# Kernel tuning notes

Hardware: AMD Instinct MI355X
Metric: run time of the kernel (lower is better)

## Reference

```python
import jax, jax.numpy as jnp
import numpy as np
import math

B, NQ, NK = 32, 1024, 1024
DQ = DK = DV = 512
H = 8
EPS = 1e-5


def _layernorm(x, g, b):
    mu = jnp.mean(x, axis=-1, keepdims=True)
    var = jnp.mean(jnp.square(x - mu), axis=-1, keepdims=True)
    return (x - mu) * jax.lax.rsqrt(var + EPS) * g + b


def setup_inputs() -> dict:
    key = jax.random.key(0)
    ks = jax.random.split(key, 8)
    s = 0.03  # small init scale for linear weights
    return {
        "Q": jax.random.normal(ks[0], (B, NQ, DQ), jnp.float32),
        "K": jax.random.normal(ks[1], (B, NK, DK), jnp.float32),
        "Wq": jax.random.normal(ks[2], (DQ, DV), jnp.float32) * s,
        "bq": jnp.zeros((DV,), jnp.float32),
        "Wk": jax.random.normal(ks[3], (DK, DV), jnp.float32) * s,
        "bk": jnp.zeros((DV,), jnp.float32),
        "Wv": jax.random.normal(ks[4], (DK, DV), jnp.float32) * s,
        "bv": jnp.zeros((DV,), jnp.float32),
        "Wo": jax.random.normal(ks[5], (DV, DV), jnp.float32) * s,
        "bo": jnp.zeros((DV,), jnp.float32),
        "g0": jnp.ones((DV,), jnp.float32),
        "beta0": jnp.zeros((DV,), jnp.float32),
        "g1": jnp.ones((DV,), jnp.float32),
        "beta1": jnp.zeros((DV,), jnp.float32),
    }


def reference(Q, K, Wq, bq, Wk, bk, Wv, bv, Wo, bo, g0, beta0, g1, beta1):
    b, nq, _ = Q.shape
    nk = K.shape[1]
    d = DV // H  # head dim (dim_split)

    q = Q @ Wq + bq            # [B, Nq, DV]
    k = K @ Wk + bk            # [B, Nk, DV]
    v = K @ Wv + bv            # [B, Nk, DV]

    # torch.cat(x.split(d, 2), 0) == reshape to [B,N,H,d] then stack heads on batch dim
    qh = q.reshape(b, nq, H, d).transpose(2, 0, 1, 3)  # [H, B, Nq, d]
    kh = k.reshape(b, nk, H, d).transpose(2, 0, 1, 3)  # [H, B, Nk, d]
    vh = v.reshape(b, nk, H, d).transpose(2, 0, 1, 3)  # [H, B, Nk, d]

    # NOTE: scaled by sqrt(dim_V), and softmax over the QUERY axis (torch dim=1)
    scores = jnp.einsum('hbqd,hbkd->hbqk', qh, kh) / math.sqrt(DV)
    A = jax.nn.softmax(scores, axis=2)                 # over Nq (faithful to source)
    oh = qh + jnp.einsum('hbqk,hbkd->hbqd', A, vh)     # residual on Q_

    out = oh.transpose(1, 2, 0, 3).reshape(b, nq, DV)  # merge heads back
    out = _layernorm(out, g0, beta0)
    out = out + jax.nn.relu(out @ Wo + bo)
    out = _layernorm(out, g1, beta1)
    return out
```

## Files before the change

kernel.cpp:

```cpp
#include <hip/hip_runtime.h>

#define Bz  32
#define NQz 1024
#define NKz 1024
#define SCALE 0.04419417382415922f

typedef __bf16 bf16_t;
typedef bf16_t bf16x8 __attribute__((ext_vector_type(8)));
typedef bf16_t bf16x4 __attribute__((ext_vector_type(4)));
typedef float  f32x4  __attribute__((ext_vector_type(4)));

#define MFMA16(a, b, c) __builtin_amdgcn_mfma_f32_16x16x32_bf16(a, b, c, 0, 0, 0)

__global__ __launch_bounds__(256) void cvt_bf16(const float* __restrict__ Q,
                                                const float* __restrict__ K,
                                                bf16_t* __restrict__ Qb,
                                                bf16_t* __restrict__ Kb) {
  const size_t i = ((size_t)blockIdx.x * 256 + threadIdx.x) * 8;
  const float* src = blockIdx.y ? K : Q;
  bf16_t* dst = blockIdx.y ? Kb : Qb;
  float4 a = *(const float4*)(src + i);
  float4 b = *(const float4*)(src + i + 4);
  bf16x8 r;
  r[0] = (bf16_t)a.x; r[1] = (bf16_t)a.y; r[2] = (bf16_t)a.z; r[3] = (bf16_t)a.w;
  r[4] = (bf16_t)b.x; r[5] = (bf16_t)b.y; r[6] = (bf16_t)b.z; r[7] = (bf16_t)b.w;
  *(bf16x8*)(dst + i) = r;
}

__global__ void transpose_w(const float* __restrict__ W0, const float* __restrict__ W1,
                            const float* __restrict__ W2, const float* __restrict__ W3,
                            bf16_t* __restrict__ out) {
  __shared__ float tile[32][33];
  const float* W = blockIdx.z == 0 ? W0 : blockIdx.z == 1 ? W1 : blockIdx.z == 2 ? W2 : W3;
  bf16_t* o = out + (size_t)blockIdx.z * 512 * 512;
  const int n0 = blockIdx.x * 32, k0 = blockIdx.y * 32;
  const int tx = threadIdx.x, ty = threadIdx.y;
  for (int i = 0; i < 4; i++)
    tile[ty + i * 8][tx] = W[(size_t)(k0 + ty + i * 8) * 512 + n0 + tx];
  __syncthreads();
  for (int i = 0; i < 4; i++)
    o[(size_t)(n0 + ty + i * 8) * 512 + k0 + tx] = (bf16_t)tile[tx][ty + i * 8];
}

template <int MODE>
__global__ __launch_bounds__(256) void gemm_k(const bf16_t* __restrict__ A,
                                              const bf16_t* __restrict__ Wt,
                                              const float* __restrict__ bias, float mult,
                                              bf16_t* __restrict__ C) {
  __shared__ __align__(16) bf16_t As[128][40];
  __shared__ __align__(16) bf16_t Bs[128][40];
  const int t = threadIdx.x;
  const int wave = t >> 6, lane = t & 63;
  const int quad = lane >> 4, l16 = lane & 15;
  const int wm = wave & 1, wn = wave >> 1;
  const int m0 = blockIdx.x * 128, n0 = blockIdx.y * 128;
  const int r = t >> 1, half = t & 1;

  f32x4 acc[4][4] = {};

  for (int k0 = 0; k0 < 512; k0 += 32) {
    __syncthreads();
    {
      const bf16_t* ap = A + (size_t)(m0 + r) * 512 + k0 + half * 16;
      *(bf16x8*)&As[r][half * 16 + 0] = *(const bf16x8*)(ap + 0);
      *(bf16x8*)&As[r][half * 16 + 8] = *(const bf16x8*)(ap + 8);
      const bf16_t* bp = Wt + (size_t)(n0 + r) * 512 + k0 + half * 16;
      *(bf16x8*)&Bs[r][half * 16 + 0] = *(const bf16x8*)(bp + 0);
      *(bf16x8*)&Bs[r][half * 16 + 8] = *(const bf16x8*)(bp + 8);
    }
    __syncthreads();
    bf16x8 af[4], bfv[4];
    for (int mt = 0; mt < 4; mt++)
      af[mt] = *(const bf16x8*)&As[wm * 64 + mt * 16 + l16][quad * 8];
    for (int nt = 0; nt < 4; nt++)
      bfv[nt] = *(const bf16x8*)&Bs[wn * 64 + nt * 16 + l16][quad * 8];
    for (int mt = 0; mt < 4; mt++)
      for (int nt = 0; nt < 4; nt++)
        acc[mt][nt] = MFMA16(af[mt], bfv[nt], acc[mt][nt]);
  }

  for (int mt = 0; mt < 4; mt++) {
    for (int nt = 0; nt < 4; nt++) {
      const int row = m0 + wm * 64 + mt * 16 + quad * 4;
      const int col = n0 + wn * 64 + nt * 16 + l16;
      const float bv = bias[col];
      for (int rg = 0; rg < 4; rg++) {
        float v = acc[mt][nt][rg] + bv;
        if (MODE == 0) {
          C[(size_t)(row + rg) * 512 + col] = (bf16_t)(v * mult);
        } else {
          float x = (float)A[(size_t)(row + rg) * 512 + col];
          C[(size_t)(row + rg) * 512 + col] = (bf16_t)(x + fmaxf(v, 0.f));
        }
      }
    }
  }
}

__global__ __launch_bounds__(256) void attn_stats(const bf16_t* __restrict__ qp,
                                                  const bf16_t* __restrict__ kp,
                                                  const bf16_t* __restrict__ vp,
                                                  bf16_t* __restrict__ Vt) {
  __shared__ __align__(16) bf16_t Vs[128][72];
  __shared__ __align__(16) bf16_t Qs[64][72];
  __shared__ float ls[128];
  const int t = threadIdx.x;
  const int wave = t >> 6, lane = t & 63;
  const int quad = lane >> 4, l16 = lane & 15;
  const int id = blockIdx.x;
  const int kb = ((id >> 3) & 7) * 128;
  const int hb = (id & 7) * 32 + (id >> 6);
  const int h = hb >> 5, b = hb & 31;
  const bf16_t* qbase = qp + (size_t)b * NQz * 512 + h * 64;
  const bf16_t* kbase = kp + (size_t)b * NKz * 512 + h * 64;

  {
    const int r = t >> 1, half = t & 1;
    const bf16_t* vr = vp + (size_t)b * NKz * 512 + (size_t)(kb + r) * 512 + h * 64 + half * 32;
    *(bf16x8*)&Vs[r][half * 32 + 0]  = *(const bf16x8*)(vr + 0);
    *(bf16x8*)&Vs[r][half * 32 + 8]  = *(const bf16x8*)(vr + 8);
    *(bf16x8*)&Vs[r][half * 32 + 16] = *(const bf16x8*)(vr + 16);
    *(bf16x8*)&Vs[r][half * 32 + 24] = *(const bf16x8*)(vr + 24);
  }

  bf16x8 aK[2][2];
  for (int mt = 0; mt < 2; mt++) {
    const bf16_t* kr = kbase + (size_t)(kb + wave * 32 + mt * 16 + l16) * 512 + quad * 8;
    aK[mt][0] = *(const bf16x8*)kr;
    aK[mt][1] = *(const bf16x8*)(kr + 32);
  }

  const int sr = t >> 2, sc = (t & 3) * 16;
  f32x4 lacc[2] = {};
  for (int q0 = 0; q0 < NQz; q0 += 64) {
    __syncthreads();
    {
      const bf16_t* qrr = qbase + (size_t)(q0 + sr) * 512 + sc;
      *(bf16x8*)&Qs[sr][sc + 0] = *(const bf16x8*)(qrr + 0);
      *(bf16x8*)&Qs[sr][sc + 8] = *(const bf16x8*)(qrr + 8);
    }
    __syncthreads();
    for (int nt = 0; nt < 4; nt++) {
      bf16x8 b0 = *(const bf16x8*)&Qs[nt * 16 + l16][quad * 8];
      bf16x8 b1 = *(const bf16x8*)&Qs[nt * 16 + l16][quad * 8 + 32];
      for (int mt = 0; mt < 2; mt++) {
        f32x4 s = {0.f, 0.f, 0.f, 0.f};
        s = MFMA16(aK[mt][0], b0, s);
        s = MFMA16(aK[mt][1], b1, s);
        lacc[mt][0] += __expf(s[0]);
        lacc[mt][1] += __expf(s[1]);
        lacc[mt][2] += __expf(s[2]);
        lacc[mt][3] += __expf(s[3]);
      }
    }
  }
  for (int mt = 0; mt < 2; mt++) {
    for (int rg = 0; rg < 4; rg++) {
      float v = lacc[mt][rg];
      v += __shfl_xor(v, 1);
      v += __shfl_xor(v, 2);
      v += __shfl_xor(v, 4);
      v += __shfl_xor(v, 8);
      if (l16 == 0) ls[wave * 32 + mt * 16 + quad * 4 + rg] = 1.0f / v;
    }
  }
  __syncthreads();
  const int d = t >> 2, kc = (t & 3) * 32;
  bf16_t* vtr = Vt + (size_t)hb * 64 * 1024 + (size_t)d * 1024 + kb + kc;
  for (int c = 0; c < 4; c++) {
    bf16x8 o;
    for (int j = 0; j < 8; j++)
      o[j] = (bf16_t)((float)Vs[kc + c * 8 + j][d] * ls[kc + c * 8 + j]);
    *(bf16x8*)(vtr + c * 8) = o;
  }
}

__global__ __launch_bounds__(256) void attn_out(const bf16_t* __restrict__ qp,
                                                const bf16_t* __restrict__ kp,
                                                const bf16_t* __restrict__ Vt,
                                                bf16_t* __restrict__ oh) {
  __shared__ __align__(16) bf16_t Ks[64][72];
  __shared__ __align__(16) bf16_t Vts[64][72];
  __shared__ __align__(16) bf16_t Ps[128][72];
  const int t = threadIdx.x;
  const int wave = t >> 6, lane = t & 63;
  const int quad = lane >> 4, l16 = lane & 15;
  const int id = blockIdx.x;
  const int qt = (id >> 3) & 7;
  const int hb = (id & 7) * 32 + (id >> 6);
  const int h = hb >> 5, b = hb & 31;
  const int q0 = qt * 128;
  const bf16_t* qbase = qp + (size_t)b * NQz * 512 + h * 64;
  const bf16_t* kbase = kp + (size_t)b * NKz * 512 + h * 64;
  const bf16_t* vtbase = Vt + (size_t)hb * 64 * 1024;

  bf16x8 bQ[2][2];
  for (int nt = 0; nt < 2; nt++) {
    const bf16_t* qr = qbase + (size_t)(q0 + wave * 32 + nt * 16 + l16) * 512 + quad * 8;
    bQ[nt][0] = *(const bf16x8*)qr;
    bQ[nt][1] = *(const bf16x8*)(qr + 32);
  }

  const int sr = t >> 2, sc = (t & 3) * 16;
  f32x4 acc[2][4] = {};
  for (int kk = 0; kk < NKz; kk += 64) {
    __syncthreads();
    {
      const bf16_t* krr = kbase + (size_t)(kk + sr) * 512 + sc;
      *(bf16x8*)&Ks[sr][sc + 0] = *(const bf16x8*)(krr + 0);
      *(bf16x8*)&Ks[sr][sc + 8] = *(const bf16x8*)(krr + 8);
      const bf16_t* vrr = vtbase + (size_t)sr * 1024 + kk + sc;
      *(bf16x8*)&Vts[sr][sc + 0] = *(const bf16x8*)(vrr + 0);
      *(bf16x8*)&Vts[sr][sc + 8] = *(const bf16x8*)(vrr + 8);
    }
    __syncthreads();
    for (int mt = 0; mt < 4; mt++) {
      bf16x8 a0 = *(const bf16x8*)&Ks[mt * 16 + l16][quad * 8];
      bf16x8 a1 = *(const bf16x8*)&Ks[mt * 16 + l16][quad * 8 + 32];
      for (int nt = 0; nt < 2; nt++) {
        f32x4 s = {0.f, 0.f, 0.f, 0.f};
        s = MFMA16(a0, bQ[nt][0], s);
        s = MFMA16(a1, bQ[nt][1], s);
        bf16x4 pk;
        pk[0] = (bf16_t)__expf(s[0]);
        pk[1] = (bf16_t)__expf(s[1]);
        pk[2] = (bf16_t)__expf(s[2]);
        pk[3] = (bf16_t)__expf(s[3]);
        *(bf16x4*)&Ps[wave * 32 + nt * 16 + l16][mt * 16 + quad * 4] = pk;
      }
    }
    bf16x8 aP[2][2];
    for (int mt = 0; mt < 2; mt++) {
      aP[mt][0] = *(const bf16x8*)&Ps[wave * 32 + mt * 16 + l16][quad * 8];
      aP[mt][1] = *(const bf16x8*)&Ps[wave * 32 + mt * 16 + l16][quad * 8 + 32];
    }
    for (int nd = 0; nd < 4; nd++) {
      bf16x8 b0 = *(const bf16x8*)&Vts[nd * 16 + l16][quad * 8];
      bf16x8 b1 = *(const bf16x8*)&Vts[nd * 16 + l16][quad * 8 + 32];
      for (int mt = 0; mt < 2; mt++) {
        acc[mt][nd] = MFMA16(aP[mt][0], b0, acc[mt][nd]);
        acc[mt][nd] = MFMA16(aP[mt][1], b1, acc[mt][nd]);
      }
    }
  }
  for (int mt = 0; mt < 2; mt++)
    for (int nd = 0; nd < 4; nd++)
      for (int rg = 0; rg < 4; rg++)
        Ps[wave * 32 + mt * 16 + quad * 4 + rg][nd * 16 + l16] = (bf16_t)acc[mt][nd][rg];
  const int row = wave * 32 + (lane >> 1), cc = (lane & 1) * 32;
  bf16_t* orow = oh + ((size_t)b * NQz + q0 + row) * 512 + h * 64 + cc;
  for (int c = 0; c < 4; c++)
    *(bf16x8*)(orow + c * 8) = *(const bf16x8*)&Ps[row][cc + c * 8];
}

template <int RES, int F32OUT>
__global__ __launch_bounds__(256) void ln_k(const bf16_t* __restrict__ x,
                                            const bf16_t* __restrict__ res,
                                            const float* __restrict__ g,
                                            const float* __restrict__ be,
                                            bf16_t* __restrict__ yb,
                                            float* __restrict__ yf) {
  const int wave = threadIdx.x >> 6, lane = threadIdx.x & 63;
  const size_t row = (size_t)blockIdx.x * 4 + wave;
  bf16x8 xv = *(const bf16x8*)(x + row * 512 + lane * 8);
  float xf[8];
  for (int i = 0; i < 8; i++) xf[i] = (float)xv[i];
  if (RES) {
    bf16x8 rv = *(const bf16x8*)(res + row * 512 + lane * 8);
    for (int i = 0; i < 8; i++) xf[i] += (float)rv[i];
  }
  float s = 0.f, sq = 0.f;
  for (int i = 0; i < 8; i++) { s += xf[i]; sq += xf[i] * xf[i]; }
  for (int off = 1; off < 64; off <<= 1) {
    s += __shfl_xor(s, off);
    sq += __shfl_xor(sq, off);
  }
  const float mu = s * (1.0f / 512.0f);
  const float var = sq * (1.0f / 512.0f) - mu * mu;
  const float rstd = rsqrtf(var + 1e-5f);
  float4 gv0 = *(const float4*)(g + lane * 8);
  float4 gv1 = *(const float4*)(g + lane * 8 + 4);
  float4 bv0 = *(const float4*)(be + lane * 8);
  float4 bv1 = *(const float4*)(be + lane * 8 + 4);
  float gg[8] = {gv0.x, gv0.y, gv0.z, gv0.w, gv1.x, gv1.y, gv1.z, gv1.w};
  float bb[8] = {bv0.x, bv0.y, bv0.z, bv0.w, bv1.x, bv1.y, bv1.z, bv1.w};
  float o[8];
  for (int i = 0; i < 8; i++) o[i] = (xf[i] - mu) * rstd * gg[i] + bb[i];
  if (F32OUT) {
    float4 o0 = {o[0], o[1], o[2], o[3]}, o1 = {o[4], o[5], o[6], o[7]};
    *(float4*)(yf + row * 512 + lane * 8) = o0;
    *(float4*)(yf + row * 512 + lane * 8 + 4) = o1;
  } else {
    bf16x8 ov;
    for (int i = 0; i < 8; i++) ov[i] = (bf16_t)o[i];
    *(bf16x8*)(yb + row * 512 + lane * 8) = ov;
  }
}

extern "C" void kernel_launch(void* const* d_in, const int* in_sizes, int n_in,
                              void* d_out, int out_size, void* d_ws, size_t ws_size,
                              hipStream_t stream) {
  (void)in_sizes; (void)n_in; (void)out_size; (void)ws_size;
  const float* Q   = (const float*)d_in[0];
  const float* K   = (const float*)d_in[1];
  const float* Wq  = (const float*)d_in[2];
  const float* bq  = (const float*)d_in[3];
  const float* Wk  = (const float*)d_in[4];
  const float* bk  = (const float*)d_in[5];
  const float* Wv  = (const float*)d_in[6];
  const float* bv  = (const float*)d_in[7];
  const float* Wo  = (const float*)d_in[8];
  const float* bo  = (const float*)d_in[9];
  const float* g0  = (const float*)d_in[10];
  const float* be0 = (const float*)d_in[11];
  const float* g1  = (const float*)d_in[12];
  const float* be1 = (const float*)d_in[13];
  float* outp = (float*)d_out;

  char* w = (char*)d_ws;
  bf16_t* Wt  = (bf16_t*)w;
  bf16_t* Qb  = (bf16_t*)(w + (2ull << 20));
  bf16_t* Kb  = (bf16_t*)(w + (34ull << 20));
  bf16_t* qp  = (bf16_t*)(w + (66ull << 20));
  bf16_t* kp  = (bf16_t*)(w + (98ull << 20));
  bf16_t* vp  = (bf16_t*)(w + (130ull << 20));
  bf16_t* Vt  = Kb;
  bf16_t* ohb = Qb;
  bf16_t* x0b = vp;
  bf16_t* oh2 = kp;

  cvt_bf16<<<dim3(8192, 2), 256, 0, stream>>>(Q, K, Qb, Kb);
  transpose_w<<<dim3(16, 16, 4), dim3(32, 8), 0, stream>>>(Wq, Wk, Wv, Wo, Wt);
  gemm_k<0><<<dim3(256, 4), 256, 0, stream>>>(Qb, Wt + 0 * (1 << 18), bq, 1.0f, qp);
  gemm_k<0><<<dim3(256, 4), 256, 0, stream>>>(Kb, Wt + 1 * (1 << 18), bk, SCALE, kp);
  gemm_k<0><<<dim3(256, 4), 256, 0, stream>>>(Kb, Wt + 2 * (1 << 18), bv, 1.0f, vp);
  attn_stats<<<2048, 256, 0, stream>>>(qp, kp, vp, Vt);
  attn_out<<<2048, 256, 0, stream>>>(qp, kp, Vt, ohb);
  ln_k<1, 0><<<8192, 256, 0, stream>>>(ohb, qp, g0, be0, x0b, nullptr);
  gemm_k<1><<<dim3(256, 4), 256, 0, stream>>>(x0b, Wt + 3 * (1 << 18), bo, 1.0f, oh2);
  ln_k<0, 1><<<8192, 256, 0, stream>>>(oh2, nullptr, g1, be1, nullptr, outp);
}
```

Before: 514.5 us.

## Fuse fp32-to-bf16 conversion into projection GEMMs and use direct global-to-LDS loads

```diff
diff --git a/kernel.cpp b/kernel.cpp
--- a/kernel.cpp
+++ b/kernel.cpp
@@ -12,19 +12,17 @@
 
 #define MFMA16(a, b, c) __builtin_amdgcn_mfma_f32_16x16x32_bf16(a, b, c, 0, 0, 0)
 
-__global__ __launch_bounds__(256) void cvt_bf16(const float* __restrict__ Q,
-                                                const float* __restrict__ K,
-                                                bf16_t* __restrict__ Qb,
-                                                bf16_t* __restrict__ Kb) {
-  const size_t i = ((size_t)blockIdx.x * 256 + threadIdx.x) * 8;
-  const float* src = blockIdx.y ? K : Q;
-  bf16_t* dst = blockIdx.y ? Kb : Qb;
-  float4 a = *(const float4*)(src + i);
-  float4 b = *(const float4*)(src + i + 4);
+__device__ __forceinline__ void gll16(const void* g, void* l) {
+  __builtin_amdgcn_global_load_lds(
+      (const __attribute__((address_space(1))) void*)g,
+      (__attribute__((address_space(3))) void*)l, 16, 0, 0);
+}
+
+__device__ __forceinline__ bf16x8 cvt8(float4 a, float4 b) {
   bf16x8 r;
   r[0] = (bf16_t)a.x; r[1] = (bf16_t)a.y; r[2] = (bf16_t)a.z; r[3] = (bf16_t)a.w;
   r[4] = (bf16_t)b.x; r[5] = (bf16_t)b.y; r[6] = (bf16_t)b.z; r[7] = (bf16_t)b.w;
-  *(bf16x8*)(dst + i) = r;
+  return r;
 }
 
 __global__ void transpose_w(const float* __restrict__ W0, const float* __restrict__ W1,
@@ -42,38 +40,106 @@
     o[(size_t)(n0 + ty + i * 8) * 512 + k0 + tx] = (bf16_t)tile[tx][ty + i * 8];
 }
 
-template <int MODE>
-__global__ __launch_bounds__(256) void gemm_k(const bf16_t* __restrict__ A,
-                                              const bf16_t* __restrict__ Wt,
-                                              const float* __restrict__ bias, float mult,
-                                              bf16_t* __restrict__ C) {
+template <int DUAL>
+__global__ __launch_bounds__(256) void gemm_f32a(const float* __restrict__ A,
+                                                 const bf16_t* __restrict__ Wt,
+                                                 const float* __restrict__ b0v,
+                                                 const float* __restrict__ b1v,
+                                                 float mult0,
+                                                 bf16_t* __restrict__ C0,
+                                                 bf16_t* __restrict__ C1) {
   __shared__ __align__(16) bf16_t As[128][40];
-  __shared__ __align__(16) bf16_t Bs[128][40];
+  __shared__ __align__(16) bf16_t Bs[128 * 32];
   const int t = threadIdx.x;
   const int wave = t >> 6, lane = t & 63;
   const int quad = lane >> 4, l16 = lane & 15;
   const int wm = wave & 1, wn = wave >> 1;
   const int m0 = blockIdx.x * 128, n0 = blockIdx.y * 128;
   const int r = t >> 1, half = t & 1;
+  const int drow = lane >> 2;
+  const int dg = (lane & 3) ^ ((lane >> 3) & 3);
 
   f32x4 acc[4][4] = {};
 
   for (int k0 = 0; k0 < 512; k0 += 32) {
     __syncthreads();
+    for (int p = 0; p < 2; p++) {
+      const bf16_t* src = Wt + (size_t)(n0 + p * 64 + wave * 16 + drow) * 512 + k0 + dg * 8;
+      gll16(src, &Bs[(p * 256 + wave * 64) * 8]);
+    }
+    {
+      const float* ap = A + (size_t)(m0 + r) * 512 + k0 + half * 16;
+      float4 a0 = *(const float4*)(ap + 0);
+      float4 a1 = *(const float4*)(ap + 4);
+      float4 a2 = *(const float4*)(ap + 8);
+      float4 a3 = *(const float4*)(ap + 12);
+      *(bf16x8*)&As[r][half * 16 + 0] = cvt8(a0, a1);
+      *(bf16x8*)&As[r][half * 16 + 8] = cvt8(a2, a3);
+    }
+    __syncthreads();
+    bf16x8 af[4], bfv[4];
+    for (int mt = 0; mt < 4; mt++)
+      af[mt] = *(const bf16x8*)&As[wm * 64 + mt * 16 + l16][quad * 8];
+    for (int nt = 0; nt < 4; nt++) {
+      const int rB = wn * 64 + nt * 16 + l16;
+      bfv[nt] = *(const bf16x8*)&Bs[rB * 32 + ((quad ^ ((rB >> 1) & 3)) * 8)];
+    }
+    for (int mt = 0; mt < 4; mt++)
+      for (int nt = 0; nt < 4; nt++)
+        acc[mt][nt] = MFMA16(af[mt], bfv[nt], acc[mt][nt]);
+  }
+
+  const float* bias = (!DUAL || n0 < 512) ? b0v : b1v;
+  bf16_t* C = (!DUAL || n0 < 512) ? C0 : C1;
+  const float mult = (!DUAL || n0 < 512) ? mult0 : 1.0f;
+  const int nb = (!DUAL || n0 < 512) ? n0 : n0 - 512;
+  for (int mt = 0; mt < 4; mt++) {
+    for (int nt = 0; nt < 4; nt++) {
+      const int row = m0 + wm * 64 + mt * 16 + quad * 4;
+      const int col = nb + wn * 64 + nt * 16 + l16;
+      const float bv = bias[col];
+      for (int rg = 0; rg < 4; rg++)
+        C[(size_t)(row + rg) * 512 + col] = (bf16_t)((acc[mt][nt][rg] + bv) * mult);
+    }
+  }
+}
+
+__global__ __launch_bounds__(256) void gemm_bf16a(const bf16_t* __restrict__ A,
+                                                  const bf16_t* __restrict__ Wt,
+                                                  const float* __restrict__ bias,
+                                                  bf16_t* __restrict__ C) {
+  __shared__ __align__(16) bf16_t As[128][40];
+  __shared__ __align__(16) bf16_t Bs[128 * 32];
+  const int t = threadIdx.x;
+  const int wave = t >> 6, lane = t & 63;
+  const int quad = lane >> 4, l16 = lane & 15;
+  const int wm = wave & 1, wn = wave >> 1;
+  const int m0 = blockIdx.x * 128, n0 = blockIdx.y * 128;
+  const int r = t >> 1, half = t & 1;
+  const int drow = lane >> 2;
+  const int dg = (lane & 3) ^ ((lane >> 3) & 3);
+
+  f32x4 acc[4][4] = {};
+
+  for (int k0 = 0; k0 < 512; k0 += 32) {
+    __syncthreads();
+    for (int p = 0; p < 2; p++) {
+      const bf16_t* src = Wt + (size_t)(n0 + p * 64 + wave * 16 + drow) * 512 + k0 + dg * 8;
+      gll16(src, &Bs[(p * 256 + wave * 64) * 8]);
+    }
     {
       const bf16_t* ap = A + (size_t)(m0 + r) * 512 + k0 + half * 16;
       *(bf16x8*)&As[r][half * 16 + 0] = *(const bf16x8*)(ap + 0);
       *(bf16x8*)&As[r][half * 16 + 8] = *(const bf16x8*)(ap + 8);
-      const bf16_t* bp = Wt + (size_t)(n0 + r) * 512 + k0 + half * 16;
-      *(bf16x8*)&Bs[r][half * 16 + 0] = *(const bf16x8*)(bp + 0);
-      *(bf16x8*)&Bs[r][half * 16 + 8] = *(const bf16x8*)(bp + 8);
     }
     __syncthreads();
     bf16x8 af[4], bfv[4];
     for (int mt = 0; mt < 4; mt++)
       af[mt] = *(const bf16x8*)&As[wm * 64 + mt * 16 + l16][quad * 8];
-    for (int nt = 0; nt < 4; nt++)
-      bfv[nt] = *(const bf16x8*)&Bs[wn * 64 + nt * 16 + l16][quad * 8];
+    for (int nt = 0; nt < 4; nt++) {
+      const int rB = wn * 64 + nt * 16 + l16;
+      bfv[nt] = *(const bf16x8*)&Bs[rB * 32 + ((quad ^ ((rB >> 1) & 3)) * 8)];
+    }
     for (int mt = 0; mt < 4; mt++)
       for (int nt = 0; nt < 4; nt++)
         acc[mt][nt] = MFMA16(af[mt], bfv[nt], acc[mt][nt]);
@@ -86,12 +152,8 @@
       const float bv = bias[col];
       for (int rg = 0; rg < 4; rg++) {
         float v = acc[mt][nt][rg] + bv;
-        if (MODE == 0) {
-          C[(size_t)(row + rg) * 512 + col] = (bf16_t)(v * mult);
-        } else {
-          float x = (float)A[(size_t)(row + rg) * 512 + col];
-          C[(size_t)(row + rg) * 512 + col] = (bf16_t)(x + fmaxf(v, 0.f));
-        }
+        float x = (float)A[(size_t)(row + rg) * 512 + col];
+        C[(size_t)(row + rg) * 512 + col] = (bf16_t)(x + fmaxf(v, 0.f));
       }
     }
   }
@@ -102,7 +164,7 @@
                                                   const bf16_t* __restrict__ vp,
                                                   bf16_t* __restrict__ Vt) {
   __shared__ __align__(16) bf16_t Vs[128][72];
-  __shared__ __align__(16) bf16_t Qs[64][72];
+  __shared__ __align__(16) bf16_t Qs[64 * 64];
   __shared__ float ls[128];
   const int t = threadIdx.x;
   const int wave = t >> 6, lane = t & 63;
@@ -113,6 +175,8 @@
   const int h = hb >> 5, b = hb & 31;
   const bf16_t* qbase = qp + (size_t)b * NQz * 512 + h * 64;
   const bf16_t* kbase = kp + (size_t)b * NKz * 512 + h * 64;
+  const int drow = lane >> 3;
+  const int dg = (lane & 7) ^ drow;
 
   {
     const int r = t >> 1, half = t & 1;
@@ -130,19 +194,18 @@
     aK[mt][1] = *(const bf16x8*)(kr + 32);
   }
 
-  const int sr = t >> 2, sc = (t & 3) * 16;
   f32x4 lacc[2] = {};
   for (int q0 = 0; q0 < NQz; q0 += 64) {
     __syncthreads();
-    {
-      const bf16_t* qrr = qbase + (size_t)(q0 + sr) * 512 + sc;
-      *(bf16x8*)&Qs[sr][sc + 0] = *(const bf16x8*)(qrr + 0);
-      *(bf16x8*)&Qs[sr][sc + 8] = *(const bf16x8*)(qrr + 8);
+    for (int p = 0; p < 2; p++) {
+      const bf16_t* src = qbase + (size_t)(q0 + p * 32 + wave * 8 + drow) * 512 + dg * 8;
+      gll16(src, &Qs[(p * 256 + wave * 64) * 8]);
     }
     __syncthreads();
     for (int nt = 0; nt < 4; nt++) {
-      bf16x8 b0 = *(const bf16x8*)&Qs[nt * 16 + l16][quad * 8];
-      bf16x8 b1 = *(const bf16x8*)&Qs[nt * 16 + l16][quad * 8 + 32];
+      const int rQ = nt * 16 + l16;
+      bf16x8 b0 = *(const bf16x8*)&Qs[rQ * 64 + ((quad ^ (rQ & 7)) * 8)];
+      bf16x8 b1 = *(const bf16x8*)&Qs[rQ * 64 + (((quad + 4) ^ (rQ & 7)) * 8)];
       for (int mt = 0; mt < 2; mt++) {
         f32x4 s = {0.f, 0.f, 0.f, 0.f};
         s = MFMA16(aK[mt][0], b0, s);
@@ -179,8 +242,8 @@
                                                 const bf16_t* __restrict__ kp,
                                                 const bf16_t* __restrict__ Vt,
                                                 bf16_t* __restrict__ oh) {
-  __shared__ __align__(16) bf16_t Ks[64][72];
-  __shared__ __align__(16) bf16_t Vts[64][72];
+  __shared__ __align__(16) bf16_t Ks[64 * 64];
+  __shared__ __align__(16) bf16_t Vts[64 * 64];
   __shared__ __align__(16) bf16_t Ps[128][72];
   const int t = threadIdx.x;
   const int wave = t >> 6, lane = t & 63;
@@ -193,6 +256,8 @@
   const bf16_t* qbase = qp + (size_t)b * NQz * 512 + h * 64;
   const bf16_t* kbase = kp + (size_t)b * NKz * 512 + h * 64;
   const bf16_t* vtbase = Vt + (size_t)hb * 64 * 1024;
+  const int drow = lane >> 3;
+  const int dg = (lane & 7) ^ drow;
 
   bf16x8 bQ[2][2];
   for (int nt = 0; nt < 2; nt++) {
@@ -201,22 +266,20 @@
     bQ[nt][1] = *(const bf16x8*)(qr + 32);
   }
 
-  const int sr = t >> 2, sc = (t & 3) * 16;
   f32x4 acc[2][4] = {};
   for (int kk = 0; kk < NKz; kk += 64) {
     __syncthreads();
-    {
-      const bf16_t* krr = kbase + (size_t)(kk + sr) * 512 + sc;
-      *(bf16x8*)&Ks[sr][sc + 0] = *(const bf16x8*)(krr + 0);
-      *(bf16x8*)&Ks[sr][sc + 8] = *(const bf16x8*)(krr + 8);
-      const bf16_t* vrr = vtbase + (size_t)sr * 1024 + kk + sc;
-      *(bf16x8*)&Vts[sr][sc + 0] = *(const bf16x8*)(vrr + 0);
-      *(bf16x8*)&Vts[sr][sc + 8] = *(const bf16x8*)(vrr + 8);
+    for (int p = 0; p < 2; p++) {
+      const bf16_t* ksrc = kbase + (size_t)(kk + p * 32 + wave * 8 + drow) * 512 + dg * 8;
+      gll16(ksrc, &Ks[(p * 256 + wave * 64) * 8]);
+      const bf16_t* vsrc = vtbase + (size_t)(p * 32 + wave * 8 + drow) * 1024 + kk + dg * 8;
+      gll16(vsrc, &Vts[(p * 256 + wave * 64) * 8]);
     }
     __syncthreads();
     for (int mt = 0; mt < 4; mt++) {
-      bf16x8 a0 = *(const bf16x8*)&Ks[mt * 16 + l16][quad * 8];
-      bf16x8 a1 = *(const bf16x8*)&Ks[mt * 16 + l16][quad * 8 + 32];
+      const int rK = mt * 16 + l16;
+      bf16x8 a0 = *(const bf16x8*)&Ks[rK * 64 + ((quad ^ (rK & 7)) * 8)];
+      bf16x8 a1 = *(const bf16x8*)&Ks[rK * 64 + (((quad + 4) ^ (rK & 7)) * 8)];
       for (int nt = 0; nt < 2; nt++) {
         f32x4 s = {0.f, 0.f, 0.f, 0.f};
         s = MFMA16(a0, bQ[nt][0], s);
@@ -235,8 +298,9 @@
       aP[mt][1] = *(const bf16x8*)&Ps[wave * 32 + mt * 16 + l16][quad * 8 + 32];
     }
     for (int nd = 0; nd < 4; nd++) {
-      bf16x8 b0 = *(const bf16x8*)&Vts[nd * 16 + l16][quad * 8];
-      bf16x8 b1 = *(const bf16x8*)&Vts[nd * 16 + l16][quad * 8 + 32];
+      const int rV = nd * 16 + l16;
+      bf16x8 b0 = *(const bf16x8*)&Vts[rV * 64 + ((quad ^ (rV & 7)) * 8)];
+      bf16x8 b1 = *(const bf16x8*)&Vts[rV * 64 + (((quad + 4) ^ (rV & 7)) * 8)];
       for (int mt = 0; mt < 2; mt++) {
         acc[mt][nd] = MFMA16(aP[mt][0], b0, acc[mt][nd]);
         acc[mt][nd] = MFMA16(aP[mt][1], b1, acc[mt][nd]);
@@ -319,24 +383,20 @@
 
   char* w = (char*)d_ws;
   bf16_t* Wt  = (bf16_t*)w;
-  bf16_t* Qb  = (bf16_t*)(w + (2ull << 20));
-  bf16_t* Kb  = (bf16_t*)(w + (34ull << 20));
-  bf16_t* qp  = (bf16_t*)(w + (66ull << 20));
-  bf16_t* kp  = (bf16_t*)(w + (98ull << 20));
-  bf16_t* vp  = (bf16_t*)(w + (130ull << 20));
-  bf16_t* Vt  = Kb;
-  bf16_t* ohb = Qb;
+  bf16_t* qp  = (bf16_t*)(w + (2ull << 20));
+  bf16_t* kp  = (bf16_t*)(w + (34ull << 20));
+  bf16_t* vp  = (bf16_t*)(w + (66ull << 20));
+  bf16_t* Vt  = (bf16_t*)(w + (98ull << 20));
+  bf16_t* ohb = (bf16_t*)(w + (130ull << 20));
   bf16_t* x0b = vp;
   bf16_t* oh2 = kp;
 
-  cvt_bf16<<<dim3(8192, 2), 256, 0, stream>>>(Q, K, Qb, Kb);
   transpose_w<<<dim3(16, 16, 4), dim3(32, 8), 0, stream>>>(Wq, Wk, Wv, Wo, Wt);
-  gemm_k<0><<<dim3(256, 4), 256, 0, stream>>>(Qb, Wt + 0 * (1 << 18), bq, 1.0f, qp);
-  gemm_k<0><<<dim3(256, 4), 256, 0, stream>>>(Kb, Wt + 1 * (1 << 18), bk, SCALE, kp);
-  gemm_k<0><<<dim3(256, 4), 256, 0, stream>>>(Kb, Wt + 2 * (1 << 18), bv, 1.0f, vp);
+  gemm_f32a<0><<<dim3(256, 4), 256, 0, stream>>>(Q, Wt, bq, nullptr, 1.0f, qp, nullptr);
+  gemm_f32a<1><<<dim3(256, 8), 256, 0, stream>>>(K, Wt + (1 << 18), bk, bv, SCALE, kp, vp);
   attn_stats<<<2048, 256, 0, stream>>>(qp, kp, vp, Vt);
   attn_out<<<2048, 256, 0, stream>>>(qp, kp, Vt, ohb);
   ln_k<1, 0><<<8192, 256, 0, stream>>>(ohb, qp, g0, be0, x0b, nullptr);
-  gemm_k<1><<<dim3(256, 4), 256, 0, stream>>>(x0b, Wt + 3 * (1 << 18), bo, 1.0f, oh2);
+  gemm_bf16a<<<dim3(256, 4), 256, 0, stream>>>(x0b, Wt + 3 * (1 << 18), bo, oh2);
   ln_k<0, 1><<<8192, 256, 0, stream>>>(oh2, nullptr, g1, be1, nullptr, outp);
 }
```

Result: faster. 494.6 us (-3.9%).
